# Kernel tuning notes

Hardware: AMD Instinct MI355X
Metric: run time of the kernel (lower is better)

The kernel has to match this reference:

```python
import jax, jax.numpy as jnp
import numpy as np

H = 256  # hidden_states


def setup_inputs() -> dict:
    key = jax.random.key(0)
    ks = jax.random.split(key, 5)
    B, T, D, O = 128, 2048, 64, 32
    u = jax.random.normal(ks[0], (B, T, D), dtype=jnp.float32)
    x0 = jax.random.uniform(ks[1], (B, 1, 2 * H), dtype=jnp.float32)
    # xavier_normal with gain 0.5: std = 0.5 * sqrt(2/(fan_in+fan_out))
    std_fiz = 0.5 * np.sqrt(2.0 / ((D + H) + 3 * H))
    std_r = 0.5 * np.sqrt(2.0 / ((D + H) + H))
    kernel_fiz = jax.random.normal(ks[2], (D + H, 3 * H), dtype=jnp.float32) * std_fiz
    kernel_r = jax.random.normal(ks[3], (D + H, H), dtype=jnp.float32) * std_r
    W_out = jax.random.normal(ks[4], (H, O), dtype=jnp.float32) * (1.0 / np.sqrt(H))
    return {
        "u": u,
        "x0": x0,
        "kernel_fiz": kernel_fiz,
        "bias_fiz": jnp.zeros((3 * H,), jnp.float32),
        "kernel_r": kernel_r,
        "bias_r": jnp.zeros((H,), jnp.float32),
        "W_out": W_out,
        "b_out": jnp.zeros((O,), jnp.float32),
    }


def reference(u, x0, kernel_fiz, bias_fiz, kernel_r, bias_r, W_out, b_out):
    # u: [B, T, D]; x0: [B, 1, 2H] -> h0, c0 each [B, H]
    h0 = x0[:, 0, :H]
    c0 = x0[:, 0, H:]

    def step(carry, u_t):
        h, c = carry  # [B, H] each
        u_ = jnp.concatenate([u_t, h], axis=-1)  # [B, D+H]
        fiz = jax.nn.sigmoid(u_ @ kernel_fiz + bias_fiz)  # [B, 3H]
        f, i, z = fiz[:, :H], fiz[:, H:2 * H], fiz[:, 2 * H:]
        r = jnp.tanh(u_ @ kernel_r + bias_r)  # [B, H]
        c_new = f * c + i * r
        h_new = z * jnp.tanh(c_new)
        y = h_new @ W_out + b_out  # [B, O]
        return (h_new, c_new), y

    _, ys = jax.lax.scan(step, (h0, c0), jnp.swapaxes(u, 0, 1))  # ys: [T, B, O]
    return jnp.swapaxes(ys, 0, 1)  # [B, T, O]
```

## Files before the change

kernel.cpp:

```cpp
#include <hip/hip_runtime.h>
#include <cstdint>
#include <cstddef>


#define HH 256
#define DD 64
#define TT 2048
#define OO 32

typedef _Float16 f16x2 __attribute__((ext_vector_type(2)));

__device__ __forceinline__ f16x2 b2h(int v) { return __builtin_bit_cast(f16x2, v); }
__device__ __forceinline__ int h2b(f16x2 v) { return __builtin_bit_cast(int, v); }

#if __has_builtin(__builtin_amdgcn_fdot2)
__device__ __forceinline__ float fdot2(f16x2 a, f16x2 b, float c) {
  return __builtin_amdgcn_fdot2(a, b, c, false);
}
#else
__device__ __forceinline__ float fdot2(f16x2 a, f16x2 b, float c) {
  return fmaf((float)a.y, (float)b.y, fmaf((float)a.x, (float)b.x, c));
}
#endif

__device__ __forceinline__ float frcp(float x) { return __builtin_amdgcn_rcpf(x); }
__device__ __forceinline__ float sigm(float x)  { return frcp(1.0f + __expf(-x)); }
__device__ __forceinline__ float tanhf_(float x){ return 1.0f - 2.0f * frcp(1.0f + __expf(2.0f * x)); }

#define BAR_LGKM() do { \
  asm volatile("s_waitcnt lgkmcnt(0)" ::: "memory"); \
  __builtin_amdgcn_s_barrier(); \
  asm volatile("" ::: "memory"); \
} while (0)

template <int CTRL>
__device__ __forceinline__ float dpp_add(float x) {
  const int t = __builtin_amdgcn_mov_dpp(__builtin_bit_cast(int, x),
                                         CTRL, 0xf, 0xf, true);
  return x + __builtin_bit_cast(float, t);
}
#define XOR_ADD4(x) do { \
  x = dpp_add<0xB1>(x);   \
  x = dpp_add<0x4E>(x);   \
} while (0)

#define UOWN(X, F, I, Z, R) do { \
  int uv_[8], ov_[16]; \
  *(int4*)&uv_[0] = ((const int4*)&(X)[rq * 16])[0]; \
  *(int4*)&uv_[4] = ((const int4*)&(X)[rq * 16])[1]; \
  *(int4*)&ov_[0]  = ((const int4*)&(X)[64 + rq * 32])[0]; \
  *(int4*)&ov_[4]  = ((const int4*)&(X)[64 + rq * 32])[1]; \
  *(int4*)&ov_[8]  = ((const int4*)&(X)[64 + rq * 32])[2]; \
  *(int4*)&ov_[12] = ((const int4*)&(X)[64 + rq * 32])[3]; \
  float a0_ = 0.0f, a1_ = 0.0f, a2_ = 0.0f, a3_ = 0.0f; \
  _Pragma("unroll") for (int k_ = 0; k_ < 8; ++k_) { \
    a0_ = fdot2(b2h(w2u[ 0 + k_]), b2h(uv_[k_]), a0_); \
    a1_ = fdot2(b2h(w2u[ 8 + k_]), b2h(uv_[k_]), a1_); \
    a2_ = fdot2(b2h(w2u[16 + k_]), b2h(uv_[k_]), a2_); \
    a3_ = fdot2(b2h(w2u[24 + k_]), b2h(uv_[k_]), a3_); \
  } \
  _Pragma("unroll") for (int k_ = 0; k_ < 16; ++k_) { \
    a0_ = fdot2(b2h(w2o[ 0 + k_]), b2h(ov_[k_]), a0_); \
    a1_ = fdot2(b2h(w2o[16 + k_]), b2h(ov_[k_]), a1_); \
    a2_ = fdot2(b2h(w2o[32 + k_]), b2h(ov_[k_]), a2_); \
    a3_ = fdot2(b2h(w2o[48 + k_]), b2h(ov_[k_]), a3_); \
  } \
  F = a0_; I = a1_; Z = a2_; R = a3_; \
} while (0)

#define PDOT(X, F, I, Z, R) do { \
  int pv_[16]; \
  *(int4*)&pv_[0]  = ((const int4*)&(X)[192 + rq * 32])[0]; \
  *(int4*)&pv_[4]  = ((const int4*)&(X)[192 + rq * 32])[1]; \
  *(int4*)&pv_[8]  = ((const int4*)&(X)[192 + rq * 32])[2]; \
  *(int4*)&pv_[12] = ((const int4*)&(X)[192 + rq * 32])[3]; \
  _Pragma("unroll") for (int k_ = 0; k_ < 16; ++k_) { \
    F = fdot2(b2h(w2p[ 0 + k_]), b2h(pv_[k_]), F); \
    I = fdot2(b2h(w2p[16 + k_]), b2h(pv_[k_]), I); \
    Z = fdot2(b2h(w2p[32 + k_]), b2h(pv_[k_]), Z); \
    R = fdot2(b2h(w2p[48 + k_]), b2h(pv_[k_]), R); \
  } \
} while (0)

#define YPART(X, OUTSLOT) do { \
  const int2* hq_ = (const int2*)&(X)[64 + jc * 16]; \
  int2 h0_ = hq_[0], h1_ = hq_[1], h2_ = hq_[2], h3_ = hq_[3]; \
  const int4* wp_ = (const int4*)&wopk[(jc * 16 + o) * 8]; \
  int4 wa_ = wp_[0], wb_ = wp_[1]; \
  float ya_ = 0.0f; \
  ya_ = fdot2(b2h(wa_.x), b2h(h0_.x), ya_); \
  ya_ = fdot2(b2h(wa_.y), b2h(h0_.y), ya_); \
  ya_ = fdot2(b2h(wa_.z), b2h(h1_.x), ya_); \
  ya_ = fdot2(b2h(wa_.w), b2h(h1_.y), ya_); \
  ya_ = fdot2(b2h(wb_.x), b2h(h2_.x), ya_); \
  ya_ = fdot2(b2h(wb_.y), b2h(h2_.y), ya_); \
  ya_ = fdot2(b2h(wb_.z), b2h(h3_.x), ya_); \
  ya_ = fdot2(b2h(wb_.w), b2h(h3_.y), ya_); \
  OUTSLOT = ya_; \
} while (0)

__global__ __launch_bounds__(512, 2)
void lstm_half(const float* __restrict__ u,    const float* __restrict__ x0,
               const float* __restrict__ kfiz, const float* __restrict__ bfiz,
               const float* __restrict__ kr,   const float* __restrict__ br,
               const float* __restrict__ wout, const float* __restrict__ bout,
               float* __restrict__ out, unsigned* __restrict__ xh)
{
  const int tid = threadIdx.x;
  const int pb = blockIdx.x;
  const int g  = (pb & 7) * 16 + ((pb >> 3) & 15);
  const int hf = pb >> 7;
  const int c  = tid >> 2;
  const int rq = tid & 3;
  const int cg = hf * 128 + c;

  __shared__ __align__(16) _Float16 uh[2][320];
  __shared__ float yred[2][16][17];
  __shared__ __align__(16) int wopk[2048];

  int w2u[32], w2o[64], w2p[64];
#pragma unroll
  for (int gg = 0; gg < 4; ++gg) {
    const float* colp = (gg < 3) ? (kfiz + gg * HH + cg) : (kr + cg);
    const int cst = (gg < 3) ? 3 * HH : HH;
#pragma unroll
    for (int k = 0; k < 8; ++k) {
      f16x2 v;
      v.x = (_Float16)colp[(rq * 16 + 2 * k    ) * cst];
      v.y = (_Float16)colp[(rq * 16 + 2 * k + 1) * cst];
      w2u[gg * 8 + k] = h2b(v);
    }
#pragma unroll
    for (int k = 0; k < 16; ++k) {
      f16x2 v;
      v.x = (_Float16)colp[(DD + hf * 128 + rq * 32 + 2 * k    ) * cst];
      v.y = (_Float16)colp[(DD + hf * 128 + rq * 32 + 2 * k + 1) * cst];
      w2o[gg * 16 + k] = h2b(v);
      f16x2 w;
      w.x = (_Float16)colp[(DD + (1 - hf) * 128 + rq * 32 + 2 * k    ) * cst];
      w.y = (_Float16)colp[(DD + (1 - hf) * 128 + rq * 32 + 2 * k + 1) * cst];
      w2p[gg * 16 + k] = h2b(w);
    }
  }
  const float bf_ = bfiz[0 * HH + cg];
  const float bi_ = bfiz[1 * HH + cg];
  const float bz_ = bfiz[2 * HH + cg];
  const float br_ = br[cg];

  for (int t = tid; t < 2048; t += 512) {
    const int k = t & 7, o = (t >> 3) & 15, jc = t >> 7;
    const int pos0 = jc * 16 + 2 * k, pos1 = pos0 + 1;
    const int ch0 = (pos0 < 128) ? hf * 128 + pos0 : (1 - hf) * 128 + (pos0 - 128);
    const int ch1 = (pos1 < 128) ? hf * 128 + pos1 : (1 - hf) * 128 + (pos1 - 128);
    f16x2 v;
    v.x = (_Float16)wout[ch0 * OO + hf * 16 + o];
    v.y = (_Float16)wout[ch1 * OO + hf * 16 + o];
    wopk[t] = h2b(v);
  }
  const float bo = (tid >= 448 && tid < 464) ? bout[hf * 16 + (tid - 448)] : 0.0f;

  float cs = x0[(size_t)g * 512 + 256 + cg];
  if (tid < 256) {
    const int ch = tid;
    const int pos = ((ch >> 7) == hf ? 64 : 192) + (ch & 127);
    uh[0][pos] = (_Float16)x0[(size_t)g * 512 + ch];
  }
  if (tid >= 448) {
    uh[0][tid - 448] = (_Float16)u[(size_t)g * TT * DD + (tid - 448)];
  }
  __syncthreads();

  float af, ai, az, ar;
  UOWN(uh[0], af, ai, az, ar);

  for (int s = 0; s < TT; ++s) {
    const int cur = s & 1, nxt = cur ^ 1;

    float un = 0.0f;
    if (tid >= 192 && tid < 256 && s + 1 < TT) {
      un = u[((size_t)g * TT + s + 1) * DD + (tid - 192)];
    }

    PDOT(uh[cur], af, ai, az, ar);

    XOR_ADD4(af); XOR_ADD4(ai); XOR_ADD4(az); XOR_ADD4(ar);
    const float f0 = sigm(af + bf_), i0 = sigm(ai + bi_);
    const float z0 = sigm(az + bz_), r0 = tanhf_(ar + br_);
    cs = f0 * cs + i0 * r0;
    const float hn = z0 * tanhf_(cs);

    if (rq == 0) {
      uh[nxt][64 + c] = (_Float16)hn;
      const unsigned short hb = __builtin_bit_cast(unsigned short, (_Float16)hn);
      __hip_atomic_store(&xh[((size_t)nxt << 15) + (size_t)g * 256 + cg],
                         ((unsigned)(s + 1) << 16) | (unsigned)hb,
                         __ATOMIC_RELAXED, __HIP_MEMORY_SCOPE_AGENT);
    }
    if (tid >= 192 && tid < 256 && s + 1 < TT) {
      uh[nxt][tid - 192] = (_Float16)un;
    }
    BAR_LGKM();

    unsigned pv = 0;
    const unsigned* pf = nullptr;
    if (tid < 128) {
      pf = xh + ((size_t)nxt << 15) + (size_t)g * 256 + (1 - hf) * 128 + tid;
      asm volatile("global_load_dword %0, %1, off sc0 sc1"
                   : "=v"(pv) : "v"(pf));
    }
    if (s >= 2 && tid >= 448 && tid < 464) {
      const int o = tid - 448;
      float ssum = bo;
#pragma unroll
      for (int k = 0; k < 16; ++k) ssum += yred[nxt][o][k];
      out[((size_t)g * TT + (s - 2)) * OO + hf * 16 + o] = ssum;
    }
    if (s >= 1 && tid >= 192 && tid < 448) {
      const int idx = tid - 192;
      const int o = idx & 15, jc = idx >> 4;
      YPART(uh[cur], yred[cur][o][jc]);
    }
    if (s + 1 < TT) {
      UOWN(uh[nxt], af, ai, az, ar);
    }

    if (tid < 128) {
      asm volatile("s_waitcnt vmcnt(0)" : "+v"(pv) :: "memory");
      const unsigned want = (unsigned)(s + 1);
      while ((pv >> 16) != want)
        pv = __hip_atomic_load(pf, __ATOMIC_RELAXED, __HIP_MEMORY_SCOPE_AGENT);
      ((unsigned short*)&uh[nxt][192])[tid] = (unsigned short)(pv & 0xFFFFu);
    }
    BAR_LGKM();
  }

  if (tid >= 448 && tid < 464) {
    const int o = tid - 448;
    float ssum = bo;
#pragma unroll
    for (int k = 0; k < 16; ++k) ssum += yred[1][o][k];
    out[((size_t)g * TT + (TT - 2)) * OO + hf * 16 + o] = ssum;
  }
  if (tid >= 192 && tid < 448) {
    const int idx = tid - 192;
    const int o = idx & 15, jc = idx >> 4;
    YPART(uh[0], yred[0][o][jc]);
  }
  __syncthreads();
  if (tid >= 448 && tid < 464) {
    const int o = tid - 448;
    float ssum = bo;
#pragma unroll
    for (int k = 0; k < 16; ++k) ssum += yred[0][o][k];
    out[((size_t)g * TT + (TT - 1)) * OO + hf * 16 + o] = ssum;
  }
}

extern "C" void kernel_launch(void* const* d_in, const int* in_sizes, int n_in,
                              void* d_out, int out_size, void* d_ws, size_t ws_size,
                              hipStream_t stream) {
  const float* u    = (const float*)d_in[0];
  const float* x0   = (const float*)d_in[1];
  const float* kfiz = (const float*)d_in[2];
  const float* bfiz = (const float*)d_in[3];
  const float* kr   = (const float*)d_in[4];
  const float* br   = (const float*)d_in[5];
  const float* wout = (const float*)d_in[6];
  const float* bout = (const float*)d_in[7];
  float* out = (float*)d_out;
  unsigned* xh = (unsigned*)d_ws;
  lstm_half<<<dim3(256), dim3(512), 0, stream>>>(
      u, x0, kfiz, bfiz, kr, br, wout, bout, out, xh);
}
```

Measured before the change: 2.774 ms.

## Batch 16 sequences per block and compute LSTM gates with MFMA

Replaces per-thread fp16 dot2 gate accumulation with 16x16x32 f16 MFMA tiles, processing 16 batch rows per block and shrinking the grid from 256 to 16 blocks. Weights are held as MFMA B-fragments in registers, and the output projection also uses MFMA in one wave. Cross-block exchange of the other half's hidden state now uses vectorized 4-wide polling. This aims to cut per-step instruction count and latency, but uses far fewer CUs and lengthens each block's serial MFMA chain.

```diff
diff --git a/kernel.cpp b/kernel.cpp
--- a/kernel.cpp
+++ b/kernel.cpp
@@ -7,21 +7,17 @@
 #define DD 64
 #define TT 2048
 #define OO 32
-
-typedef _Float16 f16x2 __attribute__((ext_vector_type(2)));
-
-__device__ __forceinline__ f16x2 b2h(int v) { return __builtin_bit_cast(f16x2, v); }
-__device__ __forceinline__ int h2b(f16x2 v) { return __builtin_bit_cast(int, v); }
-
-#if __has_builtin(__builtin_amdgcn_fdot2)
-__device__ __forceinline__ float fdot2(f16x2 a, f16x2 b, float c) {
-  return __builtin_amdgcn_fdot2(a, b, c, false);
-}
-#else
-__device__ __forceinline__ float fdot2(f16x2 a, f16x2 b, float c) {
-  return fmaf((float)a.y, (float)b.y, fmaf((float)a.x, (float)b.x, c));
-}
-#endif
+#define XROW 328
+#define GI 16
+
+typedef _Float16 f16x8 __attribute__((ext_vector_type(8)));
+typedef float    f32x4 __attribute__((ext_vector_type(4)));
+typedef unsigned u32x4 __attribute__((ext_vector_type(4)));
+typedef unsigned short u16x4 __attribute__((ext_vector_type(4)));
+
+__device__ __forceinline__ f32x4 mfma16(f16x8 a, f16x8 b, f32x4 c) {
+  return __builtin_amdgcn_mfma_f32_16x16x32_f16(a, b, c, 0, 0, 0);
+}
 
 __device__ __forceinline__ float frcp(float x) { return __builtin_amdgcn_rcpf(x); }
 __device__ __forceinline__ float sigm(float x)  { return frcp(1.0f + __expf(-x)); }
@@ -33,226 +29,198 @@
   asm volatile("" ::: "memory"); \
 } while (0)
 
-template <int CTRL>
-__device__ __forceinline__ float dpp_add(float x) {
-  const int t = __builtin_amdgcn_mov_dpp(__builtin_bit_cast(int, x),
-                                         CTRL, 0xf, 0xf, true);
-  return x + __builtin_bit_cast(float, t);
-}
-#define XOR_ADD4(x) do { \
-  x = dpp_add<0xB1>(x);   \
-  x = dpp_add<0x4E>(x);   \
+__device__ __forceinline__ u32x4 ld4_sys(const unsigned* p) {
+  u32x4 v;
+  asm volatile("global_load_dwordx4 %0, %1, off sc0 sc1\n\ts_waitcnt vmcnt(0)"
+               : "=v"(v) : "v"(p) : "memory");
+  return v;
+}
+
+#define GKT(XP, KT) do { \
+  const f16x8 a_ = *(const f16x8*)&(XP)[aoff + (KT) * 32]; \
+  acc0 = mfma16(a_, wB0[KT], acc0); \
+  acc1 = mfma16(a_, wB1[KT], acc1); \
+  acc2 = mfma16(a_, wB2[KT], acc2); \
+  acc3 = mfma16(a_, wB3[KT], acc3); \
 } while (0)
 
-#define UOWN(X, F, I, Z, R) do { \
-  int uv_[8], ov_[16]; \
-  *(int4*)&uv_[0] = ((const int4*)&(X)[rq * 16])[0]; \
-  *(int4*)&uv_[4] = ((const int4*)&(X)[rq * 16])[1]; \
-  *(int4*)&ov_[0]  = ((const int4*)&(X)[64 + rq * 32])[0]; \
-  *(int4*)&ov_[4]  = ((const int4*)&(X)[64 + rq * 32])[1]; \
-  *(int4*)&ov_[8]  = ((const int4*)&(X)[64 + rq * 32])[2]; \
-  *(int4*)&ov_[12] = ((const int4*)&(X)[64 + rq * 32])[3]; \
-  float a0_ = 0.0f, a1_ = 0.0f, a2_ = 0.0f, a3_ = 0.0f; \
-  _Pragma("unroll") for (int k_ = 0; k_ < 8; ++k_) { \
-    a0_ = fdot2(b2h(w2u[ 0 + k_]), b2h(uv_[k_]), a0_); \
-    a1_ = fdot2(b2h(w2u[ 8 + k_]), b2h(uv_[k_]), a1_); \
-    a2_ = fdot2(b2h(w2u[16 + k_]), b2h(uv_[k_]), a2_); \
-    a3_ = fdot2(b2h(w2u[24 + k_]), b2h(uv_[k_]), a3_); \
-  } \
-  _Pragma("unroll") for (int k_ = 0; k_ < 16; ++k_) { \
-    a0_ = fdot2(b2h(w2o[ 0 + k_]), b2h(ov_[k_]), a0_); \
-    a1_ = fdot2(b2h(w2o[16 + k_]), b2h(ov_[k_]), a1_); \
-    a2_ = fdot2(b2h(w2o[32 + k_]), b2h(ov_[k_]), a2_); \
-    a3_ = fdot2(b2h(w2o[48 + k_]), b2h(ov_[k_]), a3_); \
-  } \
-  F = a0_; I = a1_; Z = a2_; R = a3_; \
-} while (0)
-
-#define PDOT(X, F, I, Z, R) do { \
-  int pv_[16]; \
-  *(int4*)&pv_[0]  = ((const int4*)&(X)[192 + rq * 32])[0]; \
-  *(int4*)&pv_[4]  = ((const int4*)&(X)[192 + rq * 32])[1]; \
-  *(int4*)&pv_[8]  = ((const int4*)&(X)[192 + rq * 32])[2]; \
-  *(int4*)&pv_[12] = ((const int4*)&(X)[192 + rq * 32])[3]; \
-  _Pragma("unroll") for (int k_ = 0; k_ < 16; ++k_) { \
-    F = fdot2(b2h(w2p[ 0 + k_]), b2h(pv_[k_]), F); \
-    I = fdot2(b2h(w2p[16 + k_]), b2h(pv_[k_]), I); \
-    Z = fdot2(b2h(w2p[32 + k_]), b2h(pv_[k_]), Z); \
-    R = fdot2(b2h(w2p[48 + k_]), b2h(pv_[k_]), R); \
-  } \
-} while (0)
-
-#define YPART(X, OUTSLOT) do { \
-  const int2* hq_ = (const int2*)&(X)[64 + jc * 16]; \
-  int2 h0_ = hq_[0], h1_ = hq_[1], h2_ = hq_[2], h3_ = hq_[3]; \
-  const int4* wp_ = (const int4*)&wopk[(jc * 16 + o) * 8]; \
-  int4 wa_ = wp_[0], wb_ = wp_[1]; \
-  float ya_ = 0.0f; \
-  ya_ = fdot2(b2h(wa_.x), b2h(h0_.x), ya_); \
-  ya_ = fdot2(b2h(wa_.y), b2h(h0_.y), ya_); \
-  ya_ = fdot2(b2h(wa_.z), b2h(h1_.x), ya_); \
-  ya_ = fdot2(b2h(wa_.w), b2h(h1_.y), ya_); \
-  ya_ = fdot2(b2h(wb_.x), b2h(h2_.x), ya_); \
-  ya_ = fdot2(b2h(wb_.y), b2h(h2_.y), ya_); \
-  ya_ = fdot2(b2h(wb_.z), b2h(h3_.x), ya_); \
-  ya_ = fdot2(b2h(wb_.w), b2h(h3_.y), ya_); \
-  OUTSLOT = ya_; \
-} while (0)
-
 __global__ __launch_bounds__(512, 2)
-void lstm_half(const float* __restrict__ u,    const float* __restrict__ x0,
+void lstm_mfma(const float* __restrict__ u,    const float* __restrict__ x0,
                const float* __restrict__ kfiz, const float* __restrict__ bfiz,
                const float* __restrict__ kr,   const float* __restrict__ br,
                const float* __restrict__ wout, const float* __restrict__ bout,
                float* __restrict__ out, unsigned* __restrict__ xh)
 {
   const int tid = threadIdx.x;
-  const int pb = blockIdx.x;
-  const int g  = (pb & 7) * 16 + ((pb >> 3) & 15);
-  const int hf = pb >> 7;
-  const int c  = tid >> 2;
-  const int rq = tid & 3;
-  const int cg = hf * 128 + c;
-
-  __shared__ __align__(16) _Float16 uh[2][320];
-  __shared__ float yred[2][16][17];
-  __shared__ __align__(16) int wopk[2048];
-
-  int w2u[32], w2o[64], w2p[64];
-#pragma unroll
-  for (int gg = 0; gg < 4; ++gg) {
-    const float* colp = (gg < 3) ? (kfiz + gg * HH + cg) : (kr + cg);
-    const int cst = (gg < 3) ? 3 * HH : HH;
-#pragma unroll
-    for (int k = 0; k < 8; ++k) {
-      f16x2 v;
-      v.x = (_Float16)colp[(rq * 16 + 2 * k    ) * cst];
-      v.y = (_Float16)colp[(rq * 16 + 2 * k + 1) * cst];
-      w2u[gg * 8 + k] = h2b(v);
-    }
-#pragma unroll
-    for (int k = 0; k < 16; ++k) {
-      f16x2 v;
-      v.x = (_Float16)colp[(DD + hf * 128 + rq * 32 + 2 * k    ) * cst];
-      v.y = (_Float16)colp[(DD + hf * 128 + rq * 32 + 2 * k + 1) * cst];
-      w2o[gg * 16 + k] = h2b(v);
-      f16x2 w;
-      w.x = (_Float16)colp[(DD + (1 - hf) * 128 + rq * 32 + 2 * k    ) * cst];
-      w.y = (_Float16)colp[(DD + (1 - hf) * 128 + rq * 32 + 2 * k + 1) * cst];
-      w2p[gg * 16 + k] = h2b(w);
-    }
-  }
-  const float bf_ = bfiz[0 * HH + cg];
-  const float bi_ = bfiz[1 * HH + cg];
-  const float bz_ = bfiz[2 * HH + cg];
-  const float br_ = br[cg];
-
-  for (int t = tid; t < 2048; t += 512) {
-    const int k = t & 7, o = (t >> 3) & 15, jc = t >> 7;
-    const int pos0 = jc * 16 + 2 * k, pos1 = pos0 + 1;
-    const int ch0 = (pos0 < 128) ? hf * 128 + pos0 : (1 - hf) * 128 + (pos0 - 128);
-    const int ch1 = (pos1 < 128) ? hf * 128 + pos1 : (1 - hf) * 128 + (pos1 - 128);
-    f16x2 v;
-    v.x = (_Float16)wout[ch0 * OO + hf * 16 + o];
-    v.y = (_Float16)wout[ch1 * OO + hf * 16 + o];
-    wopk[t] = h2b(v);
-  }
-  const float bo = (tid >= 448 && tid < 464) ? bout[hf * 16 + (tid - 448)] : 0.0f;
-
-  float cs = x0[(size_t)g * 512 + 256 + cg];
+  const int bid = blockIdx.x;
+  const int g   = bid & 7;
+  const int hf  = bid >> 3;
+  const int g16 = g * GI;
+  const int l   = tid & 63;
+  const int w   = tid >> 6;
+  const int chl = w * 16 + (l & 15);
+  const int cgl = hf * 128 + chl;
+  const int itl = (l >> 4) * 4;
+  const int aoff = (l & 15) * XROW + (l >> 4) * 8;
+  const int yoff = (l & 15) * XROW + 64 + (l >> 4) * 8;
+
+  __shared__ __align__(16) _Float16 x[2][GI * XROW];
+  __shared__ __align__(16) f16x8 wy[8][64];
+
+  f16x8 wB0[10], wB1[10], wB2[10], wB3[10];
+#pragma unroll
+  for (int kt = 0; kt < 10; ++kt) {
+    f16x8 v0, v1, v2, v3;
+#pragma unroll
+    for (int j = 0; j < 8; ++j) {
+      const int k = kt * 32 + (l >> 4) * 8 + j;
+      v0[j] = (_Float16)kfiz[(size_t)k * (3 * HH) + 0 * HH + cgl];
+      v1[j] = (_Float16)kfiz[(size_t)k * (3 * HH) + 1 * HH + cgl];
+      v2[j] = (_Float16)kfiz[(size_t)k * (3 * HH) + 2 * HH + cgl];
+      v3[j] = (_Float16)kr  [(size_t)k * HH + cgl];
+    }
+    wB0[kt] = v0; wB1[kt] = v1; wB2[kt] = v2; wB3[kt] = v3;
+  }
+  const float bf_ = bfiz[0 * HH + cgl];
+  const float bi_ = bfiz[1 * HH + cgl];
+  const float bz_ = bfiz[2 * HH + cgl];
+  const float br_ = br[cgl];
+  const float boV = bout[hf * 16 + (l & 15)];
+
+  {
+    const int kt = tid >> 6, ll = tid & 63;
+    f16x8 v;
+#pragma unroll
+    for (int j = 0; j < 8; ++j)
+      v[j] = (_Float16)wout[(size_t)(kt * 32 + (ll >> 4) * 8 + j) * OO + hf * 16 + (ll & 15)];
+    wy[kt][ll] = v;
+  }
+
+  {
+    const int it = tid >> 5, c8 = (tid & 31) * 8;
+    f16x8 h8;
+#pragma unroll
+    for (int j = 0; j < 8; ++j)
+      h8[j] = (_Float16)x0[(size_t)(g16 + it) * 512 + c8 + j];
+    *(f16x8*)&x[0][it * XROW + 64 + c8] = h8;
+  }
+  const float* up = u + ((size_t)(g16 + (tid >> 4)) * TT) * DD + (tid & 15) * 4;
   if (tid < 256) {
-    const int ch = tid;
-    const int pos = ((ch >> 7) == hf ? 64 : 192) + (ch & 127);
-    uh[0][pos] = (_Float16)x0[(size_t)g * 512 + ch];
-  }
-  if (tid >= 448) {
-    uh[0][tid - 448] = (_Float16)u[(size_t)g * TT * DD + (tid - 448)];
-  }
+    const float4 uv = *(const float4*)up;
+    u16x4 w4;
+    w4.x = __builtin_bit_cast(unsigned short, (_Float16)uv.x);
+    w4.y = __builtin_bit_cast(unsigned short, (_Float16)uv.y);
+    w4.z = __builtin_bit_cast(unsigned short, (_Float16)uv.z);
+    w4.w = __builtin_bit_cast(unsigned short, (_Float16)uv.w);
+    *(u16x4*)&x[0][(tid >> 4) * XROW + (tid & 15) * 4] = w4;
+  }
+
+  float cs[4];
+#pragma unroll
+  for (int r = 0; r < 4; ++r)
+    cs[r] = x0[(size_t)(g16 + itl + r) * 512 + 256 + cgl];
+
+  unsigned* pubp = xh + (size_t)(g16 + itl) * 256 + cgl;
+  const int pch = (1 - hf) * 128 + (tid & 31) * 4;
+  const unsigned* pfb = xh + (size_t)(g16 + (tid >> 5)) * 256 + pch;
+  const int imp_off = (tid >> 5) * XROW + 64 + pch;
+  float* outp = out + ((size_t)(g16 + itl) * TT) * OO + hf * 16 + (l & 15);
+
   __syncthreads();
 
-  float af, ai, az, ar;
-  UOWN(uh[0], af, ai, az, ar);
+  f32x4 acc0 = {0.f, 0.f, 0.f, 0.f}, acc1 = acc0, acc2 = acc0, acc3 = acc0;
+  {
+    const _Float16* xp = &x[0][0];
+    GKT(xp, 0); GKT(xp, 1);
+    if (hf == 0) { GKT(xp, 2); GKT(xp, 3); GKT(xp, 4); GKT(xp, 5); }
+    else         { GKT(xp, 6); GKT(xp, 7); GKT(xp, 8); GKT(xp, 9); }
+  }
 
   for (int s = 0; s < TT; ++s) {
     const int cur = s & 1, nxt = cur ^ 1;
-
-    float un = 0.0f;
-    if (tid >= 192 && tid < 256 && s + 1 < TT) {
-      un = u[((size_t)g * TT + s + 1) * DD + (tid - 192)];
-    }
-
-    PDOT(uh[cur], af, ai, az, ar);
-
-    XOR_ADD4(af); XOR_ADD4(ai); XOR_ADD4(az); XOR_ADD4(ar);
-    const float f0 = sigm(af + bf_), i0 = sigm(ai + bi_);
-    const float z0 = sigm(az + bz_), r0 = tanhf_(ar + br_);
-    cs = f0 * cs + i0 * r0;
-    const float hn = z0 * tanhf_(cs);
-
-    if (rq == 0) {
-      uh[nxt][64 + c] = (_Float16)hn;
-      const unsigned short hb = __builtin_bit_cast(unsigned short, (_Float16)hn);
-      __hip_atomic_store(&xh[((size_t)nxt << 15) + (size_t)g * 256 + cg],
-                         ((unsigned)(s + 1) << 16) | (unsigned)hb,
+    const _Float16* xc = &x[cur][0];
+    _Float16* xn = &x[nxt][0];
+    const size_t xoff = (size_t)nxt << 15;
+    const unsigned want = (unsigned)(s + 1);
+
+    if (hf == 0) { GKT(xc, 6); GKT(xc, 7); GKT(xc, 8); GKT(xc, 9); }
+    else         { GKT(xc, 2); GKT(xc, 3); GKT(xc, 4); GKT(xc, 5); }
+
+    float hn[4];
+#pragma unroll
+    for (int r = 0; r < 4; ++r) {
+      const float fv = sigm(acc0[r] + bf_);
+      const float iv = sigm(acc1[r] + bi_);
+      const float zv = sigm(acc2[r] + bz_);
+      const float rv = tanhf_(acc3[r] + br_);
+      cs[r] = fv * cs[r] + iv * rv;
+      hn[r] = zv * tanhf_(cs[r]);
+    }
+
+#pragma unroll
+    for (int r = 0; r < 4; ++r) {
+      const _Float16 hh = (_Float16)hn[r];
+      xn[(itl + r) * XROW + 64 + cgl] = hh;
+      __hip_atomic_store(pubp + xoff + r * 256,
+                         (want << 16) | (unsigned)__builtin_bit_cast(unsigned short, hh),
                          __ATOMIC_RELAXED, __HIP_MEMORY_SCOPE_AGENT);
     }
-    if (tid >= 192 && tid < 256 && s + 1 < TT) {
-      uh[nxt][tid - 192] = (_Float16)un;
+    if (tid < 256 && s + 1 < TT) {
+      const float4 uv = *(const float4*)&up[(size_t)(s + 1) * DD];
+      u16x4 w4;
+      w4.x = __builtin_bit_cast(unsigned short, (_Float16)uv.x);
+      w4.y = __builtin_bit_cast(unsigned short, (_Float16)uv.y);
+      w4.z = __builtin_bit_cast(unsigned short, (_Float16)uv.z);
+      w4.w = __builtin_bit_cast(unsigned short, (_Float16)uv.w);
+      *(u16x4*)&xn[(tid >> 4) * XROW + (tid & 15) * 4] = w4;
     }
     BAR_LGKM();
 
-    unsigned pv = 0;
-    const unsigned* pf = nullptr;
-    if (tid < 128) {
-      pf = xh + ((size_t)nxt << 15) + (size_t)g * 256 + (1 - hf) * 128 + tid;
-      asm volatile("global_load_dword %0, %1, off sc0 sc1"
-                   : "=v"(pv) : "v"(pf));
-    }
-    if (s >= 2 && tid >= 448 && tid < 464) {
-      const int o = tid - 448;
-      float ssum = bo;
-#pragma unroll
-      for (int k = 0; k < 16; ++k) ssum += yred[nxt][o][k];
-      out[((size_t)g * TT + (s - 2)) * OO + hf * 16 + o] = ssum;
-    }
-    if (s >= 1 && tid >= 192 && tid < 448) {
-      const int idx = tid - 192;
-      const int o = idx & 15, jc = idx >> 4;
-      YPART(uh[cur], yred[cur][o][jc]);
+    u32x4 pv;
+    asm volatile("global_load_dwordx4 %0, %1, off sc0 sc1"
+                 : "=v"(pv) : "v"(pfb + xoff));
+    if (w == 0 && s >= 1) {
+      f32x4 ay = {0.f, 0.f, 0.f, 0.f};
+#pragma unroll
+      for (int kt = 0; kt < 8; ++kt) {
+        const f16x8 a_ = *(const f16x8*)&xc[yoff + kt * 32];
+        ay = mfma16(a_, wy[kt][l], ay);
+      }
+#pragma unroll
+      for (int r = 0; r < 4; ++r)
+        outp[((size_t)r * TT + (s - 1)) * OO] = ay[r] + boV;
     }
     if (s + 1 < TT) {
-      UOWN(uh[nxt], af, ai, az, ar);
-    }
-
-    if (tid < 128) {
+      acc0 = f32x4{0.f, 0.f, 0.f, 0.f}; acc1 = acc0; acc2 = acc0; acc3 = acc0;
+      GKT(xn, 0); GKT(xn, 1);
+      if (hf == 0) { GKT(xn, 2); GKT(xn, 3); GKT(xn, 4); GKT(xn, 5); }
+      else         { GKT(xn, 6); GKT(xn, 7); GKT(xn, 8); GKT(xn, 9); }
+    }
+
+    {
       asm volatile("s_waitcnt vmcnt(0)" : "+v"(pv) :: "memory");
-      const unsigned want = (unsigned)(s + 1);
-      while ((pv >> 16) != want)
-        pv = __hip_atomic_load(pf, __ATOMIC_RELAXED, __HIP_MEMORY_SCOPE_AGENT);
-      ((unsigned short*)&uh[nxt][192])[tid] = (unsigned short)(pv & 0xFFFFu);
+      while (!((pv.x >> 16) == want && (pv.y >> 16) == want &&
+               (pv.z >> 16) == want && (pv.w >> 16) == want))
+        pv = ld4_sys(pfb + xoff);
+      u16x4 hv;
+      hv.x = (unsigned short)pv.x; hv.y = (unsigned short)pv.y;
+      hv.z = (unsigned short)pv.z; hv.w = (unsigned short)pv.w;
+      *(u16x4*)&xn[imp_off] = hv;
     }
     BAR_LGKM();
   }
 
-  if (tid >= 448 && tid < 464) {
-    const int o = tid - 448;
-    float ssum = bo;
-#pragma unroll
-    for (int k = 0; k < 16; ++k) ssum += yred[1][o][k];
-    out[((size_t)g * TT + (TT - 2)) * OO + hf * 16 + o] = ssum;
-  }
-  if (tid >= 192 && tid < 448) {
-    const int idx = tid - 192;
-    const int o = idx & 15, jc = idx >> 4;
-    YPART(uh[0], yred[0][o][jc]);
-  }
-  __syncthreads();
-  if (tid >= 448 && tid < 464) {
-    const int o = tid - 448;
-    float ssum = bo;
-#pragma unroll
-    for (int k = 0; k < 16; ++k) ssum += yred[0][o][k];
-    out[((size_t)g * TT + (TT - 1)) * OO + hf * 16 + o] = ssum;
+  if (w == 0) {
+    const _Float16* xe = &x[0][0];
+    f32x4 ay = {0.f, 0.f, 0.f, 0.f};
+#pragma unroll
+    for (int kt = 0; kt < 8; ++kt) {
+      const f16x8 a_ = *(const f16x8*)&xe[yoff + kt * 32];
+      ay = mfma16(a_, wy[kt][l], ay);
+    }
+#pragma unroll
+    for (int r = 0; r < 4; ++r)
+      outp[((size_t)r * TT + (TT - 1)) * OO] = ay[r] + boV;
   }
 }
 
@@ -269,6 +237,6 @@
   const float* bout = (const float*)d_in[7];
   float* out = (float*)d_out;
   unsigned* xh = (unsigned*)d_ws;
-  lstm_half<<<dim3(256), dim3(512), 0, stream>>>(
+  lstm_mfma<<<dim3(16), dim3(512), 0, stream>>>(
       u, x0, kfiz, bfiz, kr, br, wout, bout, out, xh);
 }
```

After: 3.691 ms. 33.0% more time.
